# Performance work log

Measured on AMD Instinct MI355X. Metric: run time of the kernel, lower is better.

Reference implementation:

```python
import jax, jax.numpy as jnp
import numpy as np
import math

E = 512
H = 2048
P = 128  # attention_limit

def _make_params(key):
    ks = jax.random.split(key, 6)
    s = 0.02
    p = {}
    p['wq'] = jax.random.normal(ks[0], (E, E), jnp.float32) * s
    p['bq'] = jnp.zeros((E,), jnp.float32)
    p['wk'] = jax.random.normal(ks[1], (E, E), jnp.float32) * s
    p['bk'] = jnp.zeros((E,), jnp.float32)
    p['wv'] = jax.random.normal(ks[2], (E, E), jnp.float32) * s
    p['bv'] = jnp.zeros((E,), jnp.float32)
    p['w1'] = jax.random.normal(ks[3], (E, H), jnp.float32) * s
    p['b1'] = jnp.zeros((H,), jnp.float32)
    p['w2'] = jax.random.normal(ks[4], (H, E), jnp.float32) * s
    p['b2'] = jnp.zeros((E,), jnp.float32)
    p['ln1_w'] = jnp.ones((E,), jnp.float32)
    p['ln1_b'] = jnp.zeros((E,), jnp.float32)
    p['ln2_w'] = jnp.ones((E,), jnp.float32)
    p['ln2_b'] = jnp.zeros((E,), jnp.float32)
    return p

def setup_inputs() -> dict:
    key = jax.random.key(0)
    kx, kp = jax.random.split(key)
    inp = {'x': jax.random.normal(kx, (2, 1024, E), jnp.float32)}
    inp.update(_make_params(kp))
    return inp

def _layernorm(x, w, b, eps=1e-5):
    mu = jnp.mean(x, axis=-1, keepdims=True)
    var = jnp.mean((x - mu) ** 2, axis=-1, keepdims=True)
    return (x - mu) / jnp.sqrt(var + eps) * w + b

def _forward(x, wq, bq, wk, bk, wv, bv, w1, b1, w2, b2, ln1_w, ln1_b, ln2_w, ln2_b):
    B, S, Ed = x.shape
    # "RoPE" is actually additive sinusoidal PE in the source
    pos = jnp.arange(S, dtype=jnp.float32)[:, None]
    div = jnp.exp(jnp.arange(0, Ed, 2, dtype=jnp.float32) * (-math.log(10000.0) / Ed))
    pe = jnp.zeros((S, Ed), jnp.float32)
    pe = pe.at[:, 0::2].set(jnp.sin(pos * div))
    pe = pe.at[:, 1::2].set(jnp.cos(pos * div))
    x = x + pe[None]

    # local attention: pad x first, then apply K/V linears (padded rows -> bias)
    x_ext = jnp.pad(x, ((0, 0), (P, P), (0, 0)))
    q = x @ wq + bq                      # [B,S,E]
    k_ext = x_ext @ wk + bk              # [B,S+2P,E]
    v_ext = x_ext @ wv + bv
    W = 2 * P + 1
    win_idx = jnp.arange(S)[:, None] + jnp.arange(W)[None, :]  # [S,W]
    k_win = k_ext[:, win_idx]            # [B,S,W,E]
    v_win = v_ext[:, win_idx]            # [B,S,W,E]
    energy = jnp.einsum('bse,bswe->bsw', q, k_win) / jnp.sqrt(jnp.float32(Ed))
    attn = jax.nn.softmax(energy, axis=-1)
    attn_out = jnp.einsum('bsw,bswe->bse', attn, v_win)

    x = _layernorm(attn_out + x, ln1_w, ln1_b)
    ff = jnp.maximum(x @ w1 + b1, 0.0) @ w2 + b2
    return _layernorm(ff + x, ln2_w, ln2_b)

def reference(x, wq, bq, wk, bk, wv, bv, w1, b1, w2, b2, ln1_w, ln1_b, ln2_w, ln2_b):
    return _forward(x, wq, bq, wk, bk, wv, bv, w1, b1, w2, b2, ln1_w, ln1_b, ln2_w, ln2_b)
```

## Files before the change

kernel.cpp:

```cpp
#include <hip/hip_runtime.h>
#include <hip/hip_bf16.h>

#define S_LEN 1024
#define E_DIM 512
#define H_DIM 2048
#define P_PAD 128
#define EXTA 1296
#define BS_ROWS 2048

typedef __attribute__((ext_vector_type(8))) short bf16x8;
typedef __attribute__((ext_vector_type(4))) float f32x4;

__device__ inline ushort f2bf(float x) {
  union { float f; unsigned u; } c; c.f = x;
  unsigned u = c.u;
  u += 0x7fffu + ((u >> 16) & 1u);
  return (ushort)(u >> 16);
}

__device__ inline void gload16(ushort* dst, const ushort* src) {
  __builtin_amdgcn_global_load_lds(
      (const __attribute__((address_space(1))) void*)src,
      (__attribute__((address_space(3))) void*)dst, 16, 0, 0);
}

__global__ __launch_bounds__(256) void prep_kernel(const float* __restrict__ x,
                                                   const float* __restrict__ bk,
                                                   const float* __restrict__ bv,
                                                   const float* __restrict__ wq,
                                                   const float* __restrict__ wk,
                                                   const float* __restrict__ wv,
                                                   const float* __restrict__ w1,
                                                   const float* __restrict__ w2,
                                                   float* __restrict__ xpe,
                                                   ushort* __restrict__ xpe_bf,
                                                   ushort* __restrict__ k_bf,
                                                   ushort* __restrict__ v_t,
                                                   ushort* __restrict__ wqkvT,
                                                   ushort* __restrict__ w1T,
                                                   ushort* __restrict__ w2T) {
  __shared__ float t[32][33];
  const int blk = blockIdx.x;
  if (blk < 4096) {
    int idx = blk * 256 + threadIdx.x;
    int e = idx & (E_DIM - 1);
    int s = (idx >> 9) & (S_LEN - 1);
    const float c = -9.210340371976184f / 512.0f;
    float freq = expf((float)(e & ~1) * c);
    float ang = (float)s * freq;
    float pe = (e & 1) ? cosf(ang) : sinf(ang);
    float v = x[idx] + pe;
    xpe[idx] = v;
    xpe_bf[idx] = f2bf(v);
  } else if (blk < 6272) {
    int p = (blk - 4096) * 256 + threadIdx.x;
    int t2 = p / (2 * 272 * 512);
    int r2 = p % (2 * 272 * 512);
    int b = r2 / (272 * 512);
    int r3 = r2 % (272 * 512);
    if (t2 == 0) {
      int rr = r3 >> 9, e = r3 & 511;
      int row = rr < 128 ? rr : 1024 + rr;
      float v = rr < 256 ? bk[e] : 0.f;
      k_bf[((size_t)b * EXTA + row) * 512 + e] = f2bf(v);
    } else {
      int n = r3 / 272, jj = r3 % 272;
      int j = jj < 128 ? jj : 1024 + jj;
      float v = jj < 256 ? bv[n] : 0.f;
      v_t[((size_t)b * 512 + n) * EXTA + j] = f2bf(v);
    }
  } else {
    const int tile = blk - 6272;
    const float* W; ushort* WT; int K, N, bx, by;
    if (tile < 768) {
      K = 512; N = 512;
      int sect = tile >> 8, tt = tile & 255;
      W = sect == 0 ? wq : (sect == 1 ? wk : wv);
      WT = wqkvT + (size_t)sect * 512 * 512;
      bx = tt & 15; by = tt >> 4;
    } else if (tile < 1792) {
      K = 512; N = 2048; W = w1; WT = w1T;
      int tt = tile - 768; bx = tt & 63; by = tt >> 6;
    } else {
      K = 2048; N = 512; W = w2; WT = w2T;
      int tt = tile - 1792; bx = tt & 15; by = tt >> 4;
    }
    int lx = threadIdx.x & 31, ly = threadIdx.x >> 5;
    int n0 = bx * 32, k0 = by * 32;
#pragma unroll
    for (int r = 0; r < 4; ++r)
      t[ly + r * 8][lx] = W[(size_t)(k0 + ly + r * 8) * N + n0 + lx];
    __syncthreads();
#pragma unroll
    for (int r = 0; r < 4; ++r)
      WT[(size_t)(n0 + ly + r * 8) * K + k0 + lx] = f2bf(t[lx][ly + r * 8]);
  }
}

template <int BM, int BN, int WM, int WN, int OUT>
__global__ __launch_bounds__(256) void mfma_gemm(const ushort* __restrict__ A,
                                                 const ushort* __restrict__ Bt,
                                                 const float* __restrict__ bias,
                                                 const float* __restrict__ bias2,
                                                 const float* __restrict__ bias3,
                                                 void* __restrict__ Cout,
                                                 ushort* __restrict__ q_out,
                                                 ushort* __restrict__ k_out,
                                                 ushort* __restrict__ v_out,
                                                 int M, int N, int K, int LDA) {
  constexpr int WAVES_N = BN / WN;
  constexpr int FM = WM / 16, FN = WN / 16;
  __shared__ ushort As[BM * 64];
  __shared__ ushort Bs[BN * 64];
  const int tid = threadIdx.x;
  const int lane = tid & 63;
  const int w = tid >> 6;
  const int wr = w / WAVES_N, wc = w % WAVES_N;
  const int l15 = lane & 15, lhi = lane >> 4;
  const int col0 = blockIdx.x * BN, row0 = blockIdx.y * BM;
  const int koff = blockIdx.z * K;

  f32x4 acc[FM][FN] = {};

  for (int k0 = 0; k0 < K; k0 += 64) {
#pragma unroll
    for (int it = 0; it < BM / 32; ++it) {
      int u = it * 256 + tid;
      int r = u >> 3;
      int c16 = (u & 7) ^ (r & 7);
      gload16(&As[(size_t)u * 8], &A[(size_t)(row0 + r) * LDA + koff + k0 + c16 * 8]);
    }
#pragma unroll
    for (int it = 0; it < BN / 32; ++it) {
      int u = it * 256 + tid;
      int r = u >> 3;
      int c16 = (u & 7) ^ (r & 7);
      gload16(&Bs[(size_t)u * 8], &Bt[(size_t)(col0 + r) * LDA + koff + k0 + c16 * 8]);
    }
    __syncthreads();
#pragma unroll
    for (int kk = 0; kk < 2; ++kk) {
      bf16x8 af[FM], bfr[FN];
#pragma unroll
      for (int mi = 0; mi < FM; ++mi) {
        int r = wr * WM + mi * 16 + l15;
        int c16 = (kk * 4 + lhi) ^ (r & 7);
        af[mi] = *(const bf16x8*)&As[r * 64 + c16 * 8];
      }
#pragma unroll
      for (int ni = 0; ni < FN; ++ni) {
        int r = wc * WN + ni * 16 + l15;
        int c16 = (kk * 4 + lhi) ^ (r & 7);
        bfr[ni] = *(const bf16x8*)&Bs[r * 64 + c16 * 8];
      }
#pragma unroll
      for (int mi = 0; mi < FM; ++mi)
#pragma unroll
        for (int ni = 0; ni < FN; ++ni)
          acc[mi][ni] = __builtin_amdgcn_mfma_f32_16x16x32_bf16(af[mi], bfr[ni], acc[mi][ni], 0, 0, 0);
    }
    __syncthreads();
  }

#pragma unroll
  for (int mi = 0; mi < FM; ++mi) {
    int mbase = row0 + wr * WM + mi * 16 + lhi * 4;
#pragma unroll
    for (int ni = 0; ni < FN; ++ni) {
      int n = col0 + wc * WN + ni * 16 + l15;
      if constexpr (OUT == 1) {
        float b = bias[n];
        ushort* C = (ushort*)Cout;
#pragma unroll
        for (int j = 0; j < 4; ++j) C[(size_t)(mbase + j) * N + n] = f2bf(fmaxf(acc[mi][ni][j] + b, 0.f));
      } else if constexpr (OUT == 3) {
        float* C = (float*)Cout + (size_t)blockIdx.z * M * N;
#pragma unroll
        for (int j = 0; j < 4; ++j) C[(size_t)(mbase + j) * N + n] = acc[mi][ni][j];
      } else {
        int sect = n >> 9, nn = n & 511;
        float b = sect == 0 ? bias[nn] : (sect == 1 ? bias2[nn] : bias3[nn]);
        int bb = mbase >> 10;
        int s = mbase & 1023;
        if (sect == 0) {
#pragma unroll
          for (int j = 0; j < 4; ++j) q_out[(size_t)(mbase + j) * 512 + nn] = f2bf(acc[mi][ni][j] + b);
        } else if (sect == 1) {
#pragma unroll
          for (int j = 0; j < 4; ++j)
            k_out[((size_t)bb * EXTA + 128 + s + j) * 512 + nn] = f2bf(acc[mi][ni][j] + b);
        } else {
          ushort4 pk;
          pk.x = f2bf(acc[mi][ni][0] + b);
          pk.y = f2bf(acc[mi][ni][1] + b);
          pk.z = f2bf(acc[mi][ni][2] + b);
          pk.w = f2bf(acc[mi][ni][3] + b);
          *(ushort4*)&v_out[((size_t)bb * 512 + nn) * EXTA + 128 + s] = pk;
        }
      }
    }
  }
}

__global__ __launch_bounds__(512) void attn_ln1(const ushort* __restrict__ qb,
                                                const ushort* __restrict__ kb,
                                                const ushort* __restrict__ vt,
                                                const float* __restrict__ x_pe,
                                                const float* __restrict__ ln1w,
                                                const float* __restrict__ ln1b,
                                                float* __restrict__ x1,
                                                ushort* __restrict__ x1bf) {
  __shared__ float e_s[16][292];
  __shared__ ushort p_s[16][296];
  __shared__ float inv_s[16];
  __shared__ float redS[8][16];
  __shared__ float redQ[8][16];
  __shared__ float mu_s[16], rs_s[16];
  const int tid = threadIdx.x;
  const int lane = tid & 63;
  const int w = tid >> 6;
  const int l15 = lane & 15, lhi = lane >> 4;
  const int tile = blockIdx.x;
  const int b = tile >> 6;
  const int s0 = (tile & 63) * 16;
  const int base0 = b * 1024 + s0;

  const ushort* qrow = qb + (size_t)(base0 + l15) * 512 + lhi * 8;
  bf16x8 qf[16];
#pragma unroll
  for (int ks = 0; ks < 16; ++ks) qf[ks] = *(const bf16x8*)(qrow + ks * 32);

  const float scale = 0.044194173824159216f;
  const ushort* kbase = kb + (size_t)b * EXTA * 512 + (size_t)(s0 + l15) * 512 + lhi * 8;

  for (int jt = w; jt < 18; jt += 8) {
    f32x4 acc = {};
    const ushort* kp = kbase + (size_t)jt * 16 * 512;
#pragma unroll
    for (int ks = 0; ks < 16; ++ks) {
      bf16x8 kf = *(const bf16x8*)(kp + ks * 32);
      acc = __builtin_amdgcn_mfma_f32_16x16x32_bf16(qf[ks], kf, acc, 0, 0, 0);
    }
    int jc = jt * 16 + l15;
#pragma unroll
    for (int j = 0; j < 4; ++j) {
      int i = lhi * 4 + j;
      bool valid = (jc >= i) && (jc <= i + 256);
      e_s[i][jc] = valid ? acc[j] * scale : -1e30f;
    }
  }
  __syncthreads();

  {
    int r = tid >> 5, c0 = tid & 31;
    float m = -1e30f;
#pragma unroll
    for (int t = 0; t < 9; ++t) m = fmaxf(m, e_s[r][c0 + 32 * t]);
#pragma unroll
    for (int off = 1; off <= 16; off <<= 1) m = fmaxf(m, __shfl_xor(m, off));
    float s = 0.f;
#pragma unroll
    for (int t = 0; t < 9; ++t) {
      float p = __expf(e_s[r][c0 + 32 * t] - m);
      s += p;
      p_s[r][c0 + 32 * t] = f2bf(p);
    }
#pragma unroll
    for (int off = 1; off <= 16; off <<= 1) s += __shfl_xor(s, off);
    if (c0 == 0) inv_s[r] = 1.0f / s;
  }
  __syncthreads();

  bf16x8 pf[9];
#pragma unroll
  for (int ks = 0; ks < 9; ++ks) pf[ks] = *(const bf16x8*)&p_s[l15][ks * 32 + lhi * 8];
  float inv[4];
#pragma unroll
  for (int j = 0; j < 4; ++j) inv[j] = inv_s[lhi * 4 + j];

  const ushort* vbase = vt + (size_t)b * 512 * EXTA + s0 + lhi * 8;
  float val[4][4];
#pragma unroll
  for (int ni = 0; ni < 4; ++ni) {
    int n = w * 64 + ni * 16 + l15;
    f32x4 acc = {};
    const ushort* vp = vbase + (size_t)n * EXTA;
#pragma unroll
    for (int ks = 0; ks < 9; ++ks) {
      bf16x8 vf = *(const bf16x8*)(vp + ks * 32);
      acc = __builtin_amdgcn_mfma_f32_16x16x32_bf16(pf[ks], vf, acc, 0, 0, 0);
    }
#pragma unroll
    for (int j = 0; j < 4; ++j) {
      int r = lhi * 4 + j;
      val[ni][j] = acc[j] * inv[j] + x_pe[(size_t)(base0 + r) * 512 + n];
    }
  }

  float S[4], Q[4];
#pragma unroll
  for (int j = 0; j < 4; ++j) {
    S[j] = 0.f; Q[j] = 0.f;
#pragma unroll
    for (int ni = 0; ni < 4; ++ni) { S[j] += val[ni][j]; Q[j] += val[ni][j] * val[ni][j]; }
  }
#pragma unroll
  for (int off = 1; off <= 8; off <<= 1) {
#pragma unroll
    for (int j = 0; j < 4; ++j) {
      S[j] += __shfl_xor(S[j], off);
      Q[j] += __shfl_xor(Q[j], off);
    }
  }
  if (l15 == 0) {
#pragma unroll
    for (int j = 0; j < 4; ++j) { redS[w][lhi * 4 + j] = S[j]; redQ[w][lhi * 4 + j] = Q[j]; }
  }
  __syncthreads();
  if (tid < 16) {
    float sS = 0.f, sQ = 0.f;
#pragma unroll
    for (int ww = 0; ww < 8; ++ww) { sS += redS[ww][tid]; sQ += redQ[ww][tid]; }
    float mu = sS * (1.0f / 512.0f);
    float var = sQ * (1.0f / 512.0f) - mu * mu;
    mu_s[tid] = mu;
    rs_s[tid] = rsqrtf(var + 1e-5f);
  }
  __syncthreads();

#pragma unroll
  for (int ni = 0; ni < 4; ++ni) {
    int n = w * 64 + ni * 16 + l15;
    float lw = ln1w[n], lb = ln1b[n];
#pragma unroll
    for (int j = 0; j < 4; ++j) {
      int r = lhi * 4 + j;
      float o = (val[ni][j] - mu_s[r]) * rs_s[r] * lw + lb;
      x1[(size_t)(base0 + r) * 512 + n] = o;
      x1bf[(size_t)(base0 + r) * 512 + n] = f2bf(o);
    }
  }
}

__device__ inline float wave_reduce_sum(float v) {
#pragma unroll
  for (int off = 32; off >= 1; off >>= 1) v += __shfl_xor(v, off);
  return v;
}

__global__ __launch_bounds__(256) void ln_kernel(const float* __restrict__ a,
                                                 const float* __restrict__ a2,
                                                 const float* __restrict__ ab,
                                                 const float* __restrict__ rsd,
                                                 const float* __restrict__ w,
                                                 const float* __restrict__ bias,
                                                 float* __restrict__ out) {
  const int row = blockIdx.x;
  const int tid = threadIdx.x;
  __shared__ float red[8];
  const int e0 = tid * 2;
  const size_t base = (size_t)row * E_DIM + e0;
  float2 av = *(const float2*)(a + base);
  float2 rv = *(const float2*)(rsd + base);
  float x0 = av.x + rv.x, x1 = av.y + rv.y;
  {
    float2 v2 = *(const float2*)(a2 + base);
    x0 += v2.x; x1 += v2.y;
  }
  {
    float2 bb = *(const float2*)(ab + e0);
    x0 += bb.x; x1 += bb.y;
  }

  float sm = wave_reduce_sum(x0 + x1);
  if ((tid & 63) == 0) red[tid >> 6] = sm;
  __syncthreads();
  float mu = (red[0] + red[1] + red[2] + red[3]) * (1.0f / 512.0f);
  float d0 = x0 - mu, d1 = x1 - mu;
  float vs = wave_reduce_sum(d0 * d0 + d1 * d1);
  if ((tid & 63) == 0) red[4 + (tid >> 6)] = vs;
  __syncthreads();
  float var = (red[4] + red[5] + red[6] + red[7]) * (1.0f / 512.0f);
  float inv = rsqrtf(var + 1e-5f);
  float2 wv = *(const float2*)(w + e0);
  float2 bi = *(const float2*)(bias + e0);
  float o0 = d0 * inv * wv.x + bi.x;
  float o1 = d1 * inv * wv.y + bi.y;
  *(float2*)(out + base) = make_float2(o0, o1);
}

extern "C" void kernel_launch(void* const* d_in, const int* in_sizes, int n_in,
                              void* d_out, int out_size, void* d_ws, size_t ws_size,
                              hipStream_t stream) {
  const float* x    = (const float*)d_in[0];
  const float* wq   = (const float*)d_in[1];
  const float* bq   = (const float*)d_in[2];
  const float* wk   = (const float*)d_in[3];
  const float* bk   = (const float*)d_in[4];
  const float* wv   = (const float*)d_in[5];
  const float* bv   = (const float*)d_in[6];
  const float* w1   = (const float*)d_in[7];
  const float* b1   = (const float*)d_in[8];
  const float* w2   = (const float*)d_in[9];
  const float* b2   = (const float*)d_in[10];
  const float* ln1w = (const float*)d_in[11];
  const float* ln1b = (const float*)d_in[12];
  const float* ln2w = (const float*)d_in[13];
  const float* ln2b = (const float*)d_in[14];

  char* W = (char*)d_ws;
  float*  x_pe   = (float*)(W);
  ushort* xpebf  = (ushort*)(W + (4u  << 20));
  ushort* wqkvT  = (ushort*)(W + (6u  << 20));
  ushort* w1T    = (ushort*)(W + (8u  << 20));
  ushort* w2T    = (ushort*)(W + (10u << 20));
  ushort* q_bf   = (ushort*)(W + (12u << 20));
  ushort* k_bf   = (ushort*)(W + (14u << 20));
  ushort* v_t    = (ushort*)(W + (17u << 20));
  float*  x1     = (float*)(W + (20u << 20));
  ushort* x1bf   = (ushort*)(W + (24u << 20));
  ushort* ff1_bf = (ushort*)(W + (26u << 20));
  float*  ff2    = (float*)(W + (34u << 20));

  prep_kernel<<<9088, 256, 0, stream>>>(x, bk, bv, wq, wk, wv, w1, w2,
                                        x_pe, xpebf, k_bf, v_t, wqkvT, w1T, w2T);

  mfma_gemm<64, 128, 32, 64, 2><<<dim3(12, 32), 256, 0, stream>>>(
      xpebf, wqkvT, bq, bk, bv, nullptr, q_bf, k_bf, v_t, BS_ROWS, 1536, 512, 512);

  attn_ln1<<<128, 512, 0, stream>>>(q_bf, k_bf, v_t, x_pe, ln1w, ln1b, x1, x1bf);

  mfma_gemm<64, 128, 32, 64, 1><<<dim3(16, 32), 256, 0, stream>>>(
      x1bf, w1T, b1, nullptr, nullptr, ff1_bf, nullptr, nullptr, nullptr, BS_ROWS, H_DIM, 512, 512);

  mfma_gemm<64, 64, 32, 32, 3><<<dim3(8, 32, 2), 256, 0, stream>>>(
      ff1_bf, w2T, nullptr, nullptr, nullptr, ff2, nullptr, nullptr, nullptr, BS_ROWS, E_DIM, 1024, 2048);

  ln_kernel<<<BS_ROWS, 256, 0, stream>>>(ff2, ff2 + (size_t)BS_ROWS * E_DIM, b2, x1,
                                         ln2w, ln2b, (float*)d_out);
}
```

Baseline: 77.08 us.

## Use 128x128 GEMM tiles, 4-way split-K for FFN2, and halve prep PE blocks

```diff
diff --git a/kernel.cpp b/kernel.cpp
--- a/kernel.cpp
+++ b/kernel.cpp
@@ -4,7 +4,6 @@
 #define S_LEN 1024
 #define E_DIM 512
 #define H_DIM 2048
-#define P_PAD 128
 #define EXTA 1296
 #define BS_ROWS 2048
 
@@ -41,19 +40,22 @@
                                                    ushort* __restrict__ w2T) {
   __shared__ float t[32][33];
   const int blk = blockIdx.x;
-  if (blk < 4096) {
+  if (blk < 2048) {
     int idx = blk * 256 + threadIdx.x;
     int e = idx & (E_DIM - 1);
-    int s = (idx >> 9) & (S_LEN - 1);
+    int s = idx >> 9;
     const float c = -9.210340371976184f / 512.0f;
     float freq = expf((float)(e & ~1) * c);
     float ang = (float)s * freq;
     float pe = (e & 1) ? cosf(ang) : sinf(ang);
-    float v = x[idx] + pe;
-    xpe[idx] = v;
-    xpe_bf[idx] = f2bf(v);
-  } else if (blk < 6272) {
-    int p = (blk - 4096) * 256 + threadIdx.x;
+    float v0 = x[idx] + pe;
+    float v1 = x[idx + S_LEN * E_DIM] + pe;
+    xpe[idx] = v0;
+    xpe[idx + S_LEN * E_DIM] = v1;
+    xpe_bf[idx] = f2bf(v0);
+    xpe_bf[idx + S_LEN * E_DIM] = f2bf(v1);
+  } else if (blk < 4224) {
+    int p = (blk - 2048) * 256 + threadIdx.x;
     int t2 = p / (2 * 272 * 512);
     int r2 = p % (2 * 272 * 512);
     int b = r2 / (272 * 512);
@@ -70,7 +72,7 @@
       v_t[((size_t)b * 512 + n) * EXTA + j] = f2bf(v);
     }
   } else {
-    const int tile = blk - 6272;
+    const int tile = blk - 4224;
     const float* W; ushort* WT; int K, N, bx, by;
     if (tile < 768) {
       K = 512; N = 512;
@@ -97,7 +99,7 @@
   }
 }
 
-template <int BM, int BN, int WM, int WN, int OUT>
+template <int OUT>
 __global__ __launch_bounds__(256) void mfma_gemm(const ushort* __restrict__ A,
                                                  const ushort* __restrict__ Bt,
                                                  const float* __restrict__ bias,
@@ -108,71 +110,70 @@
                                                  ushort* __restrict__ k_out,
                                                  ushort* __restrict__ v_out,
                                                  int M, int N, int K, int LDA) {
-  constexpr int WAVES_N = BN / WN;
-  constexpr int FM = WM / 16, FN = WN / 16;
-  __shared__ ushort As[BM * 64];
-  __shared__ ushort Bs[BN * 64];
+  __shared__ ushort As[128 * 64];
+  __shared__ ushort Bs[128 * 64];
   const int tid = threadIdx.x;
   const int lane = tid & 63;
   const int w = tid >> 6;
-  const int wr = w / WAVES_N, wc = w % WAVES_N;
+  const int wr = w >> 1, wc = w & 1;
   const int l15 = lane & 15, lhi = lane >> 4;
-  const int col0 = blockIdx.x * BN, row0 = blockIdx.y * BM;
+  const int col0 = blockIdx.x * 128, row0 = blockIdx.y * 128;
   const int koff = blockIdx.z * K;
 
-  f32x4 acc[FM][FN] = {};
+  f32x4 acc[4][4] = {};
 
   for (int k0 = 0; k0 < K; k0 += 64) {
 #pragma unroll
-    for (int it = 0; it < BM / 32; ++it) {
+    for (int it = 0; it < 4; ++it) {
       int u = it * 256 + tid;
       int r = u >> 3;
       int c16 = (u & 7) ^ (r & 7);
-      gload16(&As[(size_t)u * 8], &A[(size_t)(row0 + r) * LDA + koff + k0 + c16 * 8]);
-    }
-#pragma unroll
-    for (int it = 0; it < BN / 32; ++it) {
+      gload16(&As[u * 8], &A[(size_t)(row0 + r) * LDA + koff + k0 + c16 * 8]);
+    }
+#pragma unroll
+    for (int it = 0; it < 4; ++it) {
       int u = it * 256 + tid;
       int r = u >> 3;
       int c16 = (u & 7) ^ (r & 7);
-      gload16(&Bs[(size_t)u * 8], &Bt[(size_t)(col0 + r) * LDA + koff + k0 + c16 * 8]);
+      gload16(&Bs[u * 8], &Bt[(size_t)(col0 + r) * LDA + koff + k0 + c16 * 8]);
     }
     __syncthreads();
 #pragma unroll
     for (int kk = 0; kk < 2; ++kk) {
-      bf16x8 af[FM], bfr[FN];
-#pragma unroll
-      for (int mi = 0; mi < FM; ++mi) {
-        int r = wr * WM + mi * 16 + l15;
+      bf16x8 af[4], bfv[4];
+#pragma unroll
+      for (int mi = 0; mi < 4; ++mi) {
+        int r = wr * 64 + mi * 16 + l15;
         int c16 = (kk * 4 + lhi) ^ (r & 7);
         af[mi] = *(const bf16x8*)&As[r * 64 + c16 * 8];
       }
 #pragma unroll
-      for (int ni = 0; ni < FN; ++ni) {
-        int r = wc * WN + ni * 16 + l15;
+      for (int ni = 0; ni < 4; ++ni) {
+        int r = wc * 64 + ni * 16 + l15;
         int c16 = (kk * 4 + lhi) ^ (r & 7);
-        bfr[ni] = *(const bf16x8*)&Bs[r * 64 + c16 * 8];
+        bfv[ni] = *(const bf16x8*)&Bs[r * 64 + c16 * 8];
       }
 #pragma unroll
-      for (int mi = 0; mi < FM; ++mi)
-#pragma unroll
-        for (int ni = 0; ni < FN; ++ni)
-          acc[mi][ni] = __builtin_amdgcn_mfma_f32_16x16x32_bf16(af[mi], bfr[ni], acc[mi][ni], 0, 0, 0);
+      for (int mi = 0; mi < 4; ++mi)
+#pragma unroll
+        for (int ni = 0; ni < 4; ++ni)
+          acc[mi][ni] = __builtin_amdgcn_mfma_f32_16x16x32_bf16(af[mi], bfv[ni], acc[mi][ni], 0, 0, 0);
     }
     __syncthreads();
   }
 
 #pragma unroll
-  for (int mi = 0; mi < FM; ++mi) {
-    int mbase = row0 + wr * WM + mi * 16 + lhi * 4;
-#pragma unroll
-    for (int ni = 0; ni < FN; ++ni) {
-      int n = col0 + wc * WN + ni * 16 + l15;
+  for (int mi = 0; mi < 4; ++mi) {
+    int mbase = row0 + wr * 64 + mi * 16 + lhi * 4;
+#pragma unroll
+    for (int ni = 0; ni < 4; ++ni) {
+      int n = col0 + wc * 64 + ni * 16 + l15;
       if constexpr (OUT == 1) {
         float b = bias[n];
         ushort* C = (ushort*)Cout;
 #pragma unroll
-        for (int j = 0; j < 4; ++j) C[(size_t)(mbase + j) * N + n] = f2bf(fmaxf(acc[mi][ni][j] + b, 0.f));
+        for (int j = 0; j < 4; ++j)
+          C[(size_t)(mbase + j) * N + n] = f2bf(fmaxf(acc[mi][ni][j] + b, 0.f));
       } else if constexpr (OUT == 3) {
         float* C = (float*)Cout + (size_t)blockIdx.z * M * N;
 #pragma unroll
@@ -184,7 +185,8 @@
         int s = mbase & 1023;
         if (sect == 0) {
 #pragma unroll
-          for (int j = 0; j < 4; ++j) q_out[(size_t)(mbase + j) * 512 + nn] = f2bf(acc[mi][ni][j] + b);
+          for (int j = 0; j < 4; ++j)
+            q_out[(size_t)(mbase + j) * 512 + nn] = f2bf(acc[mi][ni][j] + b);
         } else if (sect == 1) {
 #pragma unroll
           for (int j = 0; j < 4; ++j)
@@ -348,29 +350,26 @@
   return v;
 }
 
-__global__ __launch_bounds__(256) void ln_kernel(const float* __restrict__ a,
-                                                 const float* __restrict__ a2,
-                                                 const float* __restrict__ ab,
-                                                 const float* __restrict__ rsd,
-                                                 const float* __restrict__ w,
-                                                 const float* __restrict__ bias,
-                                                 float* __restrict__ out) {
+__global__ __launch_bounds__(256) void ln2_kernel(const float* __restrict__ parts,
+                                                  const float* __restrict__ ab,
+                                                  const float* __restrict__ rsd,
+                                                  const float* __restrict__ w,
+                                                  const float* __restrict__ bias,
+                                                  float* __restrict__ out) {
   const int row = blockIdx.x;
   const int tid = threadIdx.x;
   __shared__ float red[8];
   const int e0 = tid * 2;
   const size_t base = (size_t)row * E_DIM + e0;
-  float2 av = *(const float2*)(a + base);
+  const size_t PART = (size_t)BS_ROWS * E_DIM;
+  float2 v0 = *(const float2*)(parts + base);
+  float2 v1 = *(const float2*)(parts + PART + base);
+  float2 v2 = *(const float2*)(parts + 2 * PART + base);
+  float2 v3 = *(const float2*)(parts + 3 * PART + base);
+  float2 bb = *(const float2*)(ab + e0);
   float2 rv = *(const float2*)(rsd + base);
-  float x0 = av.x + rv.x, x1 = av.y + rv.y;
-  {
-    float2 v2 = *(const float2*)(a2 + base);
-    x0 += v2.x; x1 += v2.y;
-  }
-  {
-    float2 bb = *(const float2*)(ab + e0);
-    x0 += bb.x; x1 += bb.y;
-  }
+  float x0 = v0.x + v1.x + v2.x + v3.x + bb.x + rv.x;
+  float x1 = v0.y + v1.y + v2.y + v3.y + bb.y + rv.y;
 
   float sm = wave_reduce_sum(x0 + x1);
   if ((tid & 63) == 0) red[tid >> 6] = sm;
@@ -422,20 +421,19 @@
   ushort* ff1_bf = (ushort*)(W + (26u << 20));
   float*  ff2    = (float*)(W + (34u << 20));
 
-  prep_kernel<<<9088, 256, 0, stream>>>(x, bk, bv, wq, wk, wv, w1, w2,
+  prep_kernel<<<7040, 256, 0, stream>>>(x, bk, bv, wq, wk, wv, w1, w2,
                                         x_pe, xpebf, k_bf, v_t, wqkvT, w1T, w2T);
 
-  mfma_gemm<64, 128, 32, 64, 2><<<dim3(12, 32), 256, 0, stream>>>(
+  mfma_gemm<2><<<dim3(12, 16), 256, 0, stream>>>(
       xpebf, wqkvT, bq, bk, bv, nullptr, q_bf, k_bf, v_t, BS_ROWS, 1536, 512, 512);
 
   attn_ln1<<<128, 512, 0, stream>>>(q_bf, k_bf, v_t, x_pe, ln1w, ln1b, x1, x1bf);
 
-  mfma_gemm<64, 128, 32, 64, 1><<<dim3(16, 32), 256, 0, stream>>>(
+  mfma_gemm<1><<<dim3(16, 16), 256, 0, stream>>>(
       x1bf, w1T, b1, nullptr, nullptr, ff1_bf, nullptr, nullptr, nullptr, BS_ROWS, H_DIM, 512, 512);
 
-  mfma_gemm<64, 64, 32, 32, 3><<<dim3(8, 32, 2), 256, 0, stream>>>(
-      ff1_bf, w2T, nullptr, nullptr, nullptr, ff2, nullptr, nullptr, nullptr, BS_ROWS, E_DIM, 1024, 2048);
-
-  ln_kernel<<<BS_ROWS, 256, 0, stream>>>(ff2, ff2 + (size_t)BS_ROWS * E_DIM, b2, x1,
-                                         ln2w, ln2b, (float*)d_out);
-}
+  mfma_gemm<3><<<dim3(4, 16, 4), 256, 0, stream>>>(
+      ff1_bf, w2T, nullptr, nullptr, nullptr, ff2, nullptr, nullptr, nullptr, BS_ROWS, E_DIM, 512, 2048);
+
+  ln2_kernel<<<BS_ROWS, 256, 0, stream>>>(ff2, b2, x1, ln2w, ln2b, (float*)d_out);
+}
```

Result: slower. 86.18 us (+11.8%).

## Fuse FFN2 split-K GEMM with LayerNorm2 via atomic completion counters

Applied to the files above, without the earlier changes.

```diff
diff --git a/kernel.cpp b/kernel.cpp
--- a/kernel.cpp
+++ b/kernel.cpp
@@ -4,7 +4,6 @@
 #define S_LEN 1024
 #define E_DIM 512
 #define H_DIM 2048
-#define P_PAD 128
 #define EXTA 1296
 #define BS_ROWS 2048
 
@@ -16,6 +15,11 @@
   unsigned u = c.u;
   u += 0x7fffu + ((u >> 16) & 1u);
   return (ushort)(u >> 16);
+}
+__device__ inline float bf2f(ushort u) {
+  union { unsigned u; float f; } c;
+  c.u = ((unsigned)u) << 16;
+  return c.f;
 }
 
 __device__ inline void gload16(ushort* dst, const ushort* src) {
@@ -32,28 +36,27 @@
                                                    const float* __restrict__ wv,
                                                    const float* __restrict__ w1,
                                                    const float* __restrict__ w2,
-                                                   float* __restrict__ xpe,
                                                    ushort* __restrict__ xpe_bf,
                                                    ushort* __restrict__ k_bf,
                                                    ushort* __restrict__ v_t,
                                                    ushort* __restrict__ wqkvT,
                                                    ushort* __restrict__ w1T,
-                                                   ushort* __restrict__ w2T) {
+                                                   ushort* __restrict__ w2T,
+                                                   int* __restrict__ ctr) {
   __shared__ float t[32][33];
   const int blk = blockIdx.x;
-  if (blk < 4096) {
+  if (blk < 2048) {
     int idx = blk * 256 + threadIdx.x;
     int e = idx & (E_DIM - 1);
-    int s = (idx >> 9) & (S_LEN - 1);
+    int s = idx >> 9;
     const float c = -9.210340371976184f / 512.0f;
     float freq = expf((float)(e & ~1) * c);
     float ang = (float)s * freq;
     float pe = (e & 1) ? cosf(ang) : sinf(ang);
-    float v = x[idx] + pe;
-    xpe[idx] = v;
-    xpe_bf[idx] = f2bf(v);
-  } else if (blk < 6272) {
-    int p = (blk - 4096) * 256 + threadIdx.x;
+    xpe_bf[idx] = f2bf(x[idx] + pe);
+    xpe_bf[idx + S_LEN * E_DIM] = f2bf(x[idx + S_LEN * E_DIM] + pe);
+  } else if (blk < 4224) {
+    int p = (blk - 2048) * 256 + threadIdx.x;
     int t2 = p / (2 * 272 * 512);
     int r2 = p % (2 * 272 * 512);
     int b = r2 / (272 * 512);
@@ -69,8 +72,8 @@
       float v = jj < 256 ? bv[n] : 0.f;
       v_t[((size_t)b * 512 + n) * EXTA + j] = f2bf(v);
     }
-  } else {
-    const int tile = blk - 6272;
+  } else if (blk < 7040) {
+    const int tile = blk - 4224;
     const float* W; ushort* WT; int K, N, bx, by;
     if (tile < 768) {
       K = 512; N = 512;
@@ -94,6 +97,9 @@
 #pragma unroll
     for (int r = 0; r < 4; ++r)
       WT[(size_t)(n0 + ly + r * 8) * K + k0 + lx] = f2bf(t[lx][ly + r * 8]);
+  } else {
+    int idx = (blk - 7040) * 256 + threadIdx.x;
+    ctr[idx] = 0;
   }
 }
 
@@ -118,7 +124,6 @@
   const int wr = w / WAVES_N, wc = w % WAVES_N;
   const int l15 = lane & 15, lhi = lane >> 4;
   const int col0 = blockIdx.x * BN, row0 = blockIdx.y * BM;
-  const int koff = blockIdx.z * K;
 
   f32x4 acc[FM][FN] = {};
 
@@ -128,14 +133,14 @@
       int u = it * 256 + tid;
       int r = u >> 3;
       int c16 = (u & 7) ^ (r & 7);
-      gload16(&As[(size_t)u * 8], &A[(size_t)(row0 + r) * LDA + koff + k0 + c16 * 8]);
+      gload16(&As[(size_t)u * 8], &A[(size_t)(row0 + r) * LDA + k0 + c16 * 8]);
     }
 #pragma unroll
     for (int it = 0; it < BN / 32; ++it) {
       int u = it * 256 + tid;
       int r = u >> 3;
       int c16 = (u & 7) ^ (r & 7);
-      gload16(&Bs[(size_t)u * 8], &Bt[(size_t)(col0 + r) * LDA + koff + k0 + c16 * 8]);
+      gload16(&Bs[(size_t)u * 8], &Bt[(size_t)(col0 + r) * LDA + k0 + c16 * 8]);
     }
     __syncthreads();
 #pragma unroll
@@ -172,11 +177,8 @@
         float b = bias[n];
         ushort* C = (ushort*)Cout;
 #pragma unroll
-        for (int j = 0; j < 4; ++j) C[(size_t)(mbase + j) * N + n] = f2bf(fmaxf(acc[mi][ni][j] + b, 0.f));
-      } else if constexpr (OUT == 3) {
-        float* C = (float*)Cout + (size_t)blockIdx.z * M * N;
-#pragma unroll
-        for (int j = 0; j < 4; ++j) C[(size_t)(mbase + j) * N + n] = acc[mi][ni][j];
+        for (int j = 0; j < 4; ++j)
+          C[(size_t)(mbase + j) * N + n] = f2bf(fmaxf(acc[mi][ni][j] + b, 0.f));
       } else {
         int sect = n >> 9, nn = n & 511;
         float b = sect == 0 ? bias[nn] : (sect == 1 ? bias2[nn] : bias3[nn]);
@@ -184,7 +186,8 @@
         int s = mbase & 1023;
         if (sect == 0) {
 #pragma unroll
-          for (int j = 0; j < 4; ++j) q_out[(size_t)(mbase + j) * 512 + nn] = f2bf(acc[mi][ni][j] + b);
+          for (int j = 0; j < 4; ++j)
+            q_out[(size_t)(mbase + j) * 512 + nn] = f2bf(acc[mi][ni][j] + b);
         } else if (sect == 1) {
 #pragma unroll
           for (int j = 0; j < 4; ++j)
@@ -205,10 +208,9 @@
 __global__ __launch_bounds__(512) void attn_ln1(const ushort* __restrict__ qb,
                                                 const ushort* __restrict__ kb,
                                                 const ushort* __restrict__ vt,
-                                                const float* __restrict__ x_pe,
+                                                const ushort* __restrict__ xpe_bf,
                                                 const float* __restrict__ ln1w,
                                                 const float* __restrict__ ln1b,
-                                                float* __restrict__ x1,
                                                 ushort* __restrict__ x1bf) {
   __shared__ float e_s[16][292];
   __shared__ ushort p_s[16][296];
@@ -293,7 +295,7 @@
 #pragma unroll
     for (int j = 0; j < 4; ++j) {
       int r = lhi * 4 + j;
-      val[ni][j] = acc[j] * inv[j] + x_pe[(size_t)(base0 + r) * 512 + n];
+      val[ni][j] = acc[j] * inv[j] + bf2f(xpe_bf[(size_t)(base0 + r) * 512 + n]);
     }
   }
 
@@ -336,57 +338,124 @@
     for (int j = 0; j < 4; ++j) {
       int r = lhi * 4 + j;
       float o = (val[ni][j] - mu_s[r]) * rs_s[r] * lw + lb;
-      x1[(size_t)(base0 + r) * 512 + n] = o;
       x1bf[(size_t)(base0 + r) * 512 + n] = f2bf(o);
     }
   }
 }
 
-__device__ inline float wave_reduce_sum(float v) {
-#pragma unroll
-  for (int off = 32; off >= 1; off >>= 1) v += __shfl_xor(v, off);
-  return v;
-}
-
-__global__ __launch_bounds__(256) void ln_kernel(const float* __restrict__ a,
-                                                 const float* __restrict__ a2,
-                                                 const float* __restrict__ ab,
-                                                 const float* __restrict__ rsd,
-                                                 const float* __restrict__ w,
-                                                 const float* __restrict__ bias,
-                                                 float* __restrict__ out) {
-  const int row = blockIdx.x;
+__global__ __launch_bounds__(256) void ffn2_ln2(const ushort* __restrict__ A,
+                                                const ushort* __restrict__ Bt,
+                                                const float* __restrict__ b2,
+                                                const ushort* __restrict__ rsd_bf,
+                                                const float* __restrict__ ln2w,
+                                                const float* __restrict__ ln2b,
+                                                float* __restrict__ parts,
+                                                int* __restrict__ ctr,
+                                                float* __restrict__ out) {
+  __shared__ ushort As[64 * 64];
+  __shared__ ushort Bs[64 * 64];
+  __shared__ int finishf[64];
   const int tid = threadIdx.x;
-  __shared__ float red[8];
-  const int e0 = tid * 2;
-  const size_t base = (size_t)row * E_DIM + e0;
-  float2 av = *(const float2*)(a + base);
-  float2 rv = *(const float2*)(rsd + base);
-  float x0 = av.x + rv.x, x1 = av.y + rv.y;
-  {
-    float2 v2 = *(const float2*)(a2 + base);
-    x0 += v2.x; x1 += v2.y;
-  }
-  {
-    float2 bb = *(const float2*)(ab + e0);
-    x0 += bb.x; x1 += bb.y;
-  }
-
-  float sm = wave_reduce_sum(x0 + x1);
-  if ((tid & 63) == 0) red[tid >> 6] = sm;
+  const int lane = tid & 63;
+  const int w = tid >> 6;
+  const int wr = w >> 1, wc = w & 1;
+  const int l15 = lane & 15, lhi = lane >> 4;
+  const int col0 = blockIdx.x * 64, row0 = blockIdx.y * 64;
+  const int koff = blockIdx.z * 512;
+
+  f32x4 acc[2][2] = {};
+
+  for (int k0 = 0; k0 < 512; k0 += 64) {
+#pragma unroll
+    for (int it = 0; it < 2; ++it) {
+      int u = it * 256 + tid;
+      int r = u >> 3;
+      int c16 = (u & 7) ^ (r & 7);
+      gload16(&As[u * 8], &A[(size_t)(row0 + r) * 2048 + koff + k0 + c16 * 8]);
+    }
+#pragma unroll
+    for (int it = 0; it < 2; ++it) {
+      int u = it * 256 + tid;
+      int r = u >> 3;
+      int c16 = (u & 7) ^ (r & 7);
+      gload16(&Bs[u * 8], &Bt[(size_t)(col0 + r) * 2048 + koff + k0 + c16 * 8]);
+    }
+    __syncthreads();
+#pragma unroll
+    for (int kk = 0; kk < 2; ++kk) {
+      bf16x8 af[2], bfr[2];
+#pragma unroll
+      for (int mi = 0; mi < 2; ++mi) {
+        int r = wr * 32 + mi * 16 + l15;
+        int c16 = (kk * 4 + lhi) ^ (r & 7);
+        af[mi] = *(const bf16x8*)&As[r * 64 + c16 * 8];
+      }
+#pragma unroll
+      for (int ni = 0; ni < 2; ++ni) {
+        int r = wc * 32 + ni * 16 + l15;
+        int c16 = (kk * 4 + lhi) ^ (r & 7);
+        bfr[ni] = *(const bf16x8*)&Bs[r * 64 + c16 * 8];
+      }
+#pragma unroll
+      for (int mi = 0; mi < 2; ++mi)
+#pragma unroll
+        for (int ni = 0; ni < 2; ++ni)
+          acc[mi][ni] = __builtin_amdgcn_mfma_f32_16x16x32_bf16(af[mi], bfr[ni], acc[mi][ni], 0, 0, 0);
+    }
+    __syncthreads();
+  }
+
+  float* P = parts + (size_t)blockIdx.z * BS_ROWS * 512;
+#pragma unroll
+  for (int mi = 0; mi < 2; ++mi) {
+    int mbase = row0 + wr * 32 + mi * 16 + lhi * 4;
+#pragma unroll
+    for (int ni = 0; ni < 2; ++ni) {
+      int n = col0 + wc * 32 + ni * 16 + l15;
+#pragma unroll
+      for (int j = 0; j < 4; ++j) P[(size_t)(mbase + j) * 512 + n] = acc[mi][ni][j];
+    }
+  }
+
+  __threadfence();
   __syncthreads();
-  float mu = (red[0] + red[1] + red[2] + red[3]) * (1.0f / 512.0f);
-  float d0 = x0 - mu, d1 = x1 - mu;
-  float vs = wave_reduce_sum(d0 * d0 + d1 * d1);
-  if ((tid & 63) == 0) red[4 + (tid >> 6)] = vs;
+  if (tid < 64) {
+    int c = atomicAdd(&ctr[row0 + tid], 1);
+    finishf[tid] = (c == 31) ? 1 : 0;
+  }
   __syncthreads();
-  float var = (red[4] + red[5] + red[6] + red[7]) * (1.0f / 512.0f);
-  float inv = rsqrtf(var + 1e-5f);
-  float2 wv = *(const float2*)(w + e0);
-  float2 bi = *(const float2*)(bias + e0);
-  float o0 = d0 * inv * wv.x + bi.x;
-  float o1 = d1 * inv * wv.y + bi.y;
-  *(float2*)(out + base) = make_float2(o0, o1);
+  __threadfence();
+
+  const size_t PART = (size_t)BS_ROWS * 512;
+  for (int r = w; r < 64; r += 4) {
+    if (!finishf[r]) continue;
+    int row = row0 + r;
+    float v[8];
+    float S = 0.f, Q = 0.f;
+#pragma unroll
+    for (int j = 0; j < 8; ++j) {
+      int cidx = lane + 64 * j;
+      size_t off = (size_t)row * 512 + cidx;
+      float s0 = parts[off] + parts[PART + off] + parts[2 * PART + off] + parts[3 * PART + off];
+      s0 += b2[cidx] + bf2f(rsd_bf[off]);
+      v[j] = s0;
+      S += s0;
+      Q += s0 * s0;
+    }
+#pragma unroll
+    for (int off2 = 1; off2 <= 32; off2 <<= 1) {
+      S += __shfl_xor(S, off2);
+      Q += __shfl_xor(Q, off2);
+    }
+    float mu = S * (1.0f / 512.0f);
+    float var = Q * (1.0f / 512.0f) - mu * mu;
+    float rs = rsqrtf(var + 1e-5f);
+#pragma unroll
+    for (int j = 0; j < 8; ++j) {
+      int cidx = lane + 64 * j;
+      out[(size_t)row * 512 + cidx] = (v[j] - mu) * rs * ln2w[cidx] + ln2b[cidx];
+    }
+  }
 }
 
 extern "C" void kernel_launch(void* const* d_in, const int* in_sizes, int n_in,
@@ -409,33 +478,29 @@
   const float* ln2b = (const float*)d_in[14];
 
   char* W = (char*)d_ws;
-  float*  x_pe   = (float*)(W);
-  ushort* xpebf  = (ushort*)(W + (4u  << 20));
-  ushort* wqkvT  = (ushort*)(W + (6u  << 20));
-  ushort* w1T    = (ushort*)(W + (8u  << 20));
-  ushort* w2T    = (ushort*)(W + (10u << 20));
-  ushort* q_bf   = (ushort*)(W + (12u << 20));
-  ushort* k_bf   = (ushort*)(W + (14u << 20));
-  ushort* v_t    = (ushort*)(W + (17u << 20));
-  float*  x1     = (float*)(W + (20u << 20));
-  ushort* x1bf   = (ushort*)(W + (24u << 20));
-  ushort* ff1_bf = (ushort*)(W + (26u << 20));
-  float*  ff2    = (float*)(W + (34u << 20));
-
-  prep_kernel<<<9088, 256, 0, stream>>>(x, bk, bv, wq, wk, wv, w1, w2,
-                                        x_pe, xpebf, k_bf, v_t, wqkvT, w1T, w2T);
+  ushort* xpebf  = (ushort*)(W);
+  ushort* wqkvT  = (ushort*)(W + (2u  << 20));
+  ushort* w1T    = (ushort*)(W + (4u  << 20));
+  ushort* w2T    = (ushort*)(W + (6u  << 20));
+  ushort* q_bf   = (ushort*)(W + (8u  << 20));
+  ushort* k_bf   = (ushort*)(W + (10u << 20));
+  ushort* v_t    = (ushort*)(W + (13u << 20));
+  ushort* x1bf   = (ushort*)(W + (16u << 20));
+  ushort* ff1_bf = (ushort*)(W + (18u << 20));
+  float*  ff2    = (float*)(W + (26u << 20));
+  int*    ctr    = (int*)(W + (42u << 20));
+
+  prep_kernel<<<7048, 256, 0, stream>>>(x, bk, bv, wq, wk, wv, w1, w2,
+                                        xpebf, k_bf, v_t, wqkvT, w1T, w2T, ctr);
 
   mfma_gemm<64, 128, 32, 64, 2><<<dim3(12, 32), 256, 0, stream>>>(
       xpebf, wqkvT, bq, bk, bv, nullptr, q_bf, k_bf, v_t, BS_ROWS, 1536, 512, 512);
 
-  attn_ln1<<<128, 512, 0, stream>>>(q_bf, k_bf, v_t, x_pe, ln1w, ln1b, x1, x1bf);
+  attn_ln1<<<128, 512, 0, stream>>>(q_bf, k_bf, v_t, xpebf, ln1w, ln1b, x1bf);
 
   mfma_gemm<64, 128, 32, 64, 1><<<dim3(16, 32), 256, 0, stream>>>(
       x1bf, w1T, b1, nullptr, nullptr, ff1_bf, nullptr, nullptr, nullptr, BS_ROWS, H_DIM, 512, 512);
 
-  mfma_gemm<64, 64, 32, 32, 3><<<dim3(8, 32, 2), 256, 0, stream>>>(
-      ff1_bf, w2T, nullptr, nullptr, nullptr, ff2, nullptr, nullptr, nullptr, BS_ROWS, E_DIM, 1024, 2048);
-
-  ln_kernel<<<BS_ROWS, 256, 0, stream>>>(ff2, ff2 + (size_t)BS_ROWS * E_DIM, b2, x1,
-                                         ln2w, ln2b, (float*)d_out);
-}
+  ffn2_ln2<<<dim3(8, 32, 4), 256, 0, stream>>>(
+      ff1_bf, w2T, b2, x1bf, ln2w, ln2b, ff2, ctr, (float*)d_out);
+}
```

Result: slower. 288.4 us (+274.1%).
